# Performance work log

Hardware: AMD Instinct MI355X
Metric: run time of the kernel (lower is better)

The kernel has to match this reference:

```python
import jax, jax.numpy as jnp
import numpy as np

NEG = -1e6  # mask fill value used by d2l-style masked_softmax


def setup_inputs() -> dict:
    key = jax.random.key(0)
    kq, kk, kv, kl = jax.random.split(key, 4)
    B, Lq, Lk, D = 8, 2048, 2048, 64
    Q = jax.random.normal(kq, (B, Lq, D), dtype=jnp.float32)
    K = jax.random.normal(kk, (B, Lk, D), dtype=jnp.float32)
    V = jax.random.normal(kv, (B, Lk, D), dtype=jnp.float32)
    valid_len = jax.random.randint(kl, (B,), 1, Lk + 1, dtype=jnp.int64)
    return {"Q": Q, "K": K, "V": V, "valid_len": valid_len}


def reference(Q, K, V, valid_len):
    d = Q.shape[-1]
    scale = 1.0 / jnp.sqrt(jnp.asarray(d, dtype=Q.dtype))
    # scores: [B, Lq, Lk]
    S = jnp.einsum('bqd,bkd->bqk', Q, K) * scale
    Lk = K.shape[1]
    # per-batch key-length mask: position j valid iff j < valid_len[b]
    mask = jnp.arange(Lk)[None, None, :] < valid_len[:, None, None]
    S = jnp.where(mask, S, NEG)
    A = jax.nn.softmax(S, axis=-1)
    return jnp.einsum('bqk,bkd->bqd', A, V)
```

## Files before the change

### kernel.cpp

```cpp
#include <hip/hip_runtime.h>
#include <hip/hip_bf16.h>


constexpr int B_  = 8;
constexpr int L_  = 2048;
constexpr int D_  = 64;
constexpr int BQ  = 128;
constexpr int BK  = 64;
constexpr int LDK = 72;
constexpr int NQ  = L_ / BQ;

constexpr float QSCALE = 0.125f * 1.44269504088896340736f;

using bf16x8 = __attribute__((ext_vector_type(8))) __bf16;
using f32x4  = __attribute__((ext_vector_type(4))) float;

union frag_u { unsigned u[4]; bf16x8 v; };

#if __has_builtin(__builtin_amdgcn_exp2f)
#define EXP2(x) __builtin_amdgcn_exp2f(x)
#else
#define EXP2(x) exp2f(x)
#endif

__device__ __forceinline__ unsigned pack2(float lo, float hi) {
    __hip_bfloat162 h = __float22bfloat162_rn(make_float2(lo, hi));
    return *(unsigned*)&h;
}
__device__ __forceinline__ int sniff_valid(const int* vl, int b) {
    const int p1 = vl[1];
    return (p1 == 0) ? vl[2 * b] : vl[b];
}

__global__ __launch_bounds__(256, 3) void attn_fwd(
    const float* __restrict__ Q, const float* __restrict__ K,
    const float* __restrict__ V, const int* __restrict__ vl,
    float* __restrict__ O, float* __restrict__ Opart,
    float* __restrict__ lpart, int nsplit, int splitk)
{
    __shared__ __align__(16) unsigned short Ks[BK * LDK];
    __shared__ __align__(16) unsigned short Vt[D_ * LDK];
    __shared__ __align__(16) unsigned short Ps[4 * 32 * LDK];

    const int id   = blockIdx.x;
    const int qt   = id & (NQ - 1);
    const int b    = (id >> 4) & (B_ - 1);
    const int s    = id >> 7;
    const int tid  = threadIdx.x;
    const int wave = tid >> 6;
    const int lan  = tid & 15;
    const int quad = (tid >> 4) & 3;

    const int valid  = sniff_valid(vl, b);
    const int kstart = s * splitk;
    if (kstart >= valid) return;
    const int kend   = min(kstart + splitk, valid);
    const int ntiles = (kend - kstart + BK - 1) / BK;

    const float* Kg = K + (size_t)b * L_ * D_;
    const float* Vg = V + (size_t)b * L_ * D_;

    const int krow = tid >> 2, kc0 = (tid & 3) * 16;
    const int vk0  = (tid & 31) * 2, vd0 = (tid >> 5) * 8;

    float4 kr[4], vr[4];
    {
        const float* ks = Kg + (size_t)(kstart + krow) * D_ + kc0;
        #pragma unroll
        for (int p = 0; p < 4; ++p) kr[p] = *(const float4*)(ks + 4 * p);
        const float* vs = Vg + (size_t)(kstart + vk0) * D_ + vd0;
        vr[0] = *(const float4*)(vs);
        vr[1] = *(const float4*)(vs + 4);
        vr[2] = *(const float4*)(vs + D_);
        vr[3] = *(const float4*)(vs + D_ + 4);
    }

    bf16x8 aq[2][2];
    #pragma unroll
    for (int g = 0; g < 2; ++g) {
        const float* qs = Q + ((size_t)b * L_ + qt * BQ + wave * 32 + g * 16 + lan) * D_;
        float4 q0 = *(const float4*)(qs + quad * 8);
        float4 q1 = *(const float4*)(qs + quad * 8 + 4);
        float4 q2 = *(const float4*)(qs + 32 + quad * 8);
        float4 q3 = *(const float4*)(qs + 32 + quad * 8 + 4);
        frag_u f0, f1;
        f0.u[0] = pack2(q0.x * QSCALE, q0.y * QSCALE);
        f0.u[1] = pack2(q0.z * QSCALE, q0.w * QSCALE);
        f0.u[2] = pack2(q1.x * QSCALE, q1.y * QSCALE);
        f0.u[3] = pack2(q1.z * QSCALE, q1.w * QSCALE);
        f1.u[0] = pack2(q2.x * QSCALE, q2.y * QSCALE);
        f1.u[1] = pack2(q2.z * QSCALE, q2.w * QSCALE);
        f1.u[2] = pack2(q3.x * QSCALE, q3.y * QSCALE);
        f1.u[3] = pack2(q3.z * QSCALE, q3.w * QSCALE);
        aq[g][0] = f0.v;
        aq[g][1] = f1.v;
    }

    f32x4 oacc[2][4];
    #pragma unroll
    for (int g = 0; g < 2; ++g)
        #pragma unroll
        for (int c = 0; c < 4; ++c) oacc[g][c] = (f32x4){0.f, 0.f, 0.f, 0.f};
    float lsum[2] = {0.f, 0.f};

    unsigned short* Pw = &Ps[wave * 32 * LDK];

    for (int t = 0; t < ntiles; ++t) {
        const int kt = kstart + t * BK;
        __syncthreads();

        {
            unsigned us[8];
            #pragma unroll
            for (int p = 0; p < 4; ++p) {
                us[2*p]   = pack2(kr[p].x, kr[p].y);
                us[2*p+1] = pack2(kr[p].z, kr[p].w);
            }
            *(uint4*)&Ks[krow * LDK + kc0]     = *(uint4*)&us[0];
            *(uint4*)&Ks[krow * LDK + kc0 + 8] = *(uint4*)&us[4];
        }
        {
            const float* a = (const float*)&vr[0];
            const float* c = (const float*)&vr[2];
            #pragma unroll
            for (int j = 0; j < 8; ++j)
                *(unsigned*)&Vt[(vd0 + j) * LDK + vk0] = pack2(a[j], c[j]);
        }
        __syncthreads();

        if (t + 1 < ntiles) {
            const int kn = kt + BK;
            const float* ks = Kg + (size_t)(kn + krow) * D_ + kc0;
            #pragma unroll
            for (int p = 0; p < 4; ++p) kr[p] = *(const float4*)(ks + 4 * p);
            const float* vs = Vg + (size_t)(kn + vk0) * D_ + vd0;
            vr[0] = *(const float4*)(vs);
            vr[1] = *(const float4*)(vs + 4);
            vr[2] = *(const float4*)(vs + D_);
            vr[3] = *(const float4*)(vs + D_ + 4);
        }

        #pragma unroll
        for (int c = 0; c < 4; ++c) {
            bf16x8 ak0 = *(const bf16x8*)&Ks[(c*16 + lan) * LDK + quad * 8];
            bf16x8 ak1 = *(const bf16x8*)&Ks[(c*16 + lan) * LDK + 32 + quad * 8];
            f32x4 z0 = (f32x4){0.f, 0.f, 0.f, 0.f};
            f32x4 z1 = (f32x4){0.f, 0.f, 0.f, 0.f};
            z0 = __builtin_amdgcn_mfma_f32_16x16x32_bf16(ak0, aq[0][0], z0, 0, 0, 0);
            z1 = __builtin_amdgcn_mfma_f32_16x16x32_bf16(ak0, aq[1][0], z1, 0, 0, 0);
            z0 = __builtin_amdgcn_mfma_f32_16x16x32_bf16(ak1, aq[0][1], z0, 0, 0, 0);
            z1 = __builtin_amdgcn_mfma_f32_16x16x32_bf16(ak1, aq[1][1], z1, 0, 0, 0);

            const int kbase = kt + c * 16 + quad * 4;
            float p0[4], p1[4];
            #pragma unroll
            for (int r = 0; r < 4; ++r) {
                const bool ok = (kbase + r) < valid;
                p0[r] = ok ? EXP2(z0[r]) : 0.f;
                p1[r] = ok ? EXP2(z1[r]) : 0.f;
                lsum[0] += p0[r];
                lsum[1] += p1[r];
            }
            *(uint2*)&Pw[lan * LDK + c * 16 + quad * 4] =
                make_uint2(pack2(p0[0], p0[1]), pack2(p0[2], p0[3]));
            *(uint2*)&Pw[(16 + lan) * LDK + c * 16 + quad * 4] =
                make_uint2(pack2(p1[0], p1[1]), pack2(p1[2], p1[3]));
        }

        bf16x8 ap[2][2];
        #pragma unroll
        for (int g = 0; g < 2; ++g) {
            ap[g][0] = *(const bf16x8*)&Pw[(g*16 + lan) * LDK + quad * 8];
            ap[g][1] = *(const bf16x8*)&Pw[(g*16 + lan) * LDK + 32 + quad * 8];
        }
        #pragma unroll
        for (int c = 0; c < 4; ++c) {
            bf16x8 bv0 = *(const bf16x8*)&Vt[(c*16 + lan) * LDK + quad * 8];
            bf16x8 bv1 = *(const bf16x8*)&Vt[(c*16 + lan) * LDK + 32 + quad * 8];
            #pragma unroll
            for (int g = 0; g < 2; ++g) {
                oacc[g][c] = __builtin_amdgcn_mfma_f32_16x16x32_bf16(ap[g][0], bv0, oacc[g][c], 0, 0, 0);
                oacc[g][c] = __builtin_amdgcn_mfma_f32_16x16x32_bf16(ap[g][1], bv1, oacc[g][c], 0, 0, 0);
            }
        }
    }

    #pragma unroll
    for (int g = 0; g < 2; ++g) {
        lsum[g] += __shfl_xor(lsum[g], 16);
        lsum[g] += __shfl_xor(lsum[g], 32);
    }

    const int rowbase = qt * BQ + wave * 32;
    if (nsplit == 1) {
        #pragma unroll
        for (int g = 0; g < 2; ++g) {
            float inv[4];
            #pragma unroll
            for (int r = 0; r < 4; ++r)
                inv[r] = 1.0f / __shfl(lsum[g], quad * 4 + r);
            float* Og = O + ((size_t)b * L_ + rowbase + g * 16) * D_;
            #pragma unroll
            for (int c = 0; c < 4; ++c)
                #pragma unroll
                for (int r = 0; r < 4; ++r)
                    Og[(size_t)(quad * 4 + r) * D_ + c * 16 + lan] = oacc[g][c][r] * inv[r];
        }
    } else {
        #pragma unroll
        for (int g = 0; g < 2; ++g) {
            float* Og = Opart + ((size_t)s * B_ * L_ + (size_t)b * L_ + rowbase + g * 16) * D_;
            #pragma unroll
            for (int c = 0; c < 4; ++c)
                #pragma unroll
                for (int r = 0; r < 4; ++r)
                    Og[(size_t)(quad * 4 + r) * D_ + c * 16 + lan] = oacc[g][c][r];
            if (quad == 0)
                lpart[(size_t)s * B_ * L_ + (size_t)b * L_ + rowbase + g * 16 + lan] = lsum[g];
        }
    }
}

__global__ __launch_bounds__(256) void attn_combine(
    const float* __restrict__ Opart, const float* __restrict__ lpart,
    const int* __restrict__ vl, float* __restrict__ O,
    int nsplit, int splitk)
{
    const int idx = blockIdx.x * 256 + threadIdx.x;
    const int row = idx >> 4;
    const int b   = row >> 11;
    const int off = (idx & 15) * 4;
    const int valid = sniff_valid(vl, b);
    const int ns = min(nsplit, (valid + splitk - 1) / splitk);

    float Lsum = 0.f;
    float4 acc = make_float4(0.f, 0.f, 0.f, 0.f);
    for (int s = 0; s < ns; ++s) {
        Lsum += lpart[s * (B_ * L_) + row];
        float4 o4 = *(const float4*)&Opart[(size_t)s * (B_ * L_ * D_) + (size_t)row * D_ + off];
        acc.x += o4.x; acc.y += o4.y; acc.z += o4.z; acc.w += o4.w;
    }
    const float inv = 1.0f / Lsum;
    acc.x *= inv; acc.y *= inv; acc.z *= inv; acc.w *= inv;
    *(float4*)&O[(size_t)row * D_ + off] = acc;
}

extern "C" void kernel_launch(void* const* d_in, const int* in_sizes, int n_in,
                              void* d_out, int out_size, void* d_ws, size_t ws_size,
                              hipStream_t stream) {
    const float* Q  = (const float*)d_in[0];
    const float* K  = (const float*)d_in[1];
    const float* V  = (const float*)d_in[2];
    const int*   vl = (const int*)d_in[3];
    float* O = (float*)d_out;

    auto need = [](int n) {
        return (size_t)n * (B_ * L_ * D_ + B_ * L_) * sizeof(float);
    };
    int nsplit = 1;
    if      (ws_size >= need(4)) nsplit = 4;
    else if (ws_size >= need(2)) nsplit = 2;
    const int splitk = L_ / nsplit;

    float* Opart = (float*)d_ws;
    float* lpart = Opart + (size_t)nsplit * B_ * L_ * D_;

    attn_fwd<<<dim3(nsplit * B_ * NQ), 256, 0, stream>>>(
        Q, K, V, vl, O, Opart, lpart, nsplit, splitk);
    if (nsplit > 1)
        attn_combine<<<dim3((B_ * L_ * D_ / 4) / 256), 256, 0, stream>>>(
            Opart, lpart, vl, O, nsplit, splitk);
}
```

Measured before the change: 88.63 us.

## Fuse split-K combine into attention kernel via last-block atomic counter

Removes the separate combine kernel. Each split block writes its partial output and row sums, then bumps a per-tile atomic counter, and the last block to arrive reduces all splits and writes the final output. This saves one kernel launch and lets the reduction overlap with other blocks still computing. In exchange it adds a memset launch for the counters, thread fences, and a serialized reduction inside the final block of each tile.

Result: slower. 116.4 us (+31.4%).

```diff
diff --git a/kernel.cpp b/kernel.cpp
--- a/kernel.cpp
+++ b/kernel.cpp
@@ -36,11 +36,13 @@
     const float* __restrict__ Q, const float* __restrict__ K,
     const float* __restrict__ V, const int* __restrict__ vl,
     float* __restrict__ O, float* __restrict__ Opart,
-    float* __restrict__ lpart, int nsplit, int splitk)
+    float* __restrict__ lpart, int* __restrict__ cnt,
+    int nsplit, int splitk)
 {
     __shared__ __align__(16) unsigned short Ks[BK * LDK];
     __shared__ __align__(16) unsigned short Vt[D_ * LDK];
     __shared__ __align__(16) unsigned short Ps[4 * 32 * LDK];
+    __shared__ int last_flag;
 
     const int id   = blockIdx.x;
     const int qt   = id & (NQ - 1);
@@ -206,43 +208,48 @@
                 for (int r = 0; r < 4; ++r)
                     Og[(size_t)(quad * 4 + r) * D_ + c * 16 + lan] = oacc[g][c][r] * inv[r];
         }
-    } else {
-        #pragma unroll
-        for (int g = 0; g < 2; ++g) {
-            float* Og = Opart + ((size_t)s * B_ * L_ + (size_t)b * L_ + rowbase + g * 16) * D_;
-            #pragma unroll
-            for (int c = 0; c < 4; ++c)
-                #pragma unroll
-                for (int r = 0; r < 4; ++r)
-                    Og[(size_t)(quad * 4 + r) * D_ + c * 16 + lan] = oacc[g][c][r];
-            if (quad == 0)
-                lpart[(size_t)s * B_ * L_ + (size_t)b * L_ + rowbase + g * 16 + lan] = lsum[g];
-        }
-    }
-}
-
-__global__ __launch_bounds__(256) void attn_combine(
-    const float* __restrict__ Opart, const float* __restrict__ lpart,
-    const int* __restrict__ vl, float* __restrict__ O,
-    int nsplit, int splitk)
-{
-    const int idx = blockIdx.x * 256 + threadIdx.x;
-    const int row = idx >> 4;
-    const int b   = row >> 11;
-    const int off = (idx & 15) * 4;
-    const int valid = sniff_valid(vl, b);
+        return;
+    }
+
+    #pragma unroll
+    for (int g = 0; g < 2; ++g) {
+        float* Og = Opart + ((size_t)s * B_ * L_ + (size_t)b * L_ + rowbase + g * 16) * D_;
+        #pragma unroll
+        for (int c = 0; c < 4; ++c)
+            #pragma unroll
+            for (int r = 0; r < 4; ++r)
+                Og[(size_t)(quad * 4 + r) * D_ + c * 16 + lan] = oacc[g][c][r];
+        if (quad == 0)
+            lpart[(size_t)s * B_ * L_ + (size_t)b * L_ + rowbase + g * 16 + lan] = lsum[g];
+    }
+
     const int ns = min(nsplit, (valid + splitk - 1) / splitk);
-
-    float Lsum = 0.f;
-    float4 acc = make_float4(0.f, 0.f, 0.f, 0.f);
-    for (int s = 0; s < ns; ++s) {
-        Lsum += lpart[s * (B_ * L_) + row];
-        float4 o4 = *(const float4*)&Opart[(size_t)s * (B_ * L_ * D_) + (size_t)row * D_ + off];
-        acc.x += o4.x; acc.y += o4.y; acc.z += o4.z; acc.w += o4.w;
-    }
-    const float inv = 1.0f / Lsum;
-    acc.x *= inv; acc.y *= inv; acc.z *= inv; acc.w *= inv;
-    *(float4*)&O[(size_t)row * D_ + off] = acc;
+    __syncthreads();
+    if (tid == 0) {
+        __threadfence();
+        const int prev = atomicAdd(&cnt[b * NQ + qt], 1);
+        last_flag = (prev == ns - 1);
+    }
+    __syncthreads();
+    if (!last_flag) return;
+    __threadfence();
+
+    const size_t row0 = (size_t)b * L_ + qt * BQ;
+    for (int i = tid; i < BQ * (D_ / 4); i += 256) {
+        const int r   = i >> 4;
+        const int off = (i & 15) * 4;
+        const size_t row = row0 + r;
+        float Ls = 0.f;
+        float4 acc = make_float4(0.f, 0.f, 0.f, 0.f);
+        for (int s2 = 0; s2 < ns; ++s2) {
+            Ls += lpart[(size_t)s2 * (B_ * L_) + row];
+            float4 o4 = *(const float4*)&Opart[(size_t)s2 * (B_ * L_ * D_) + row * D_ + off];
+            acc.x += o4.x; acc.y += o4.y; acc.z += o4.z; acc.w += o4.w;
+        }
+        const float inv = 1.0f / Ls;
+        acc.x *= inv; acc.y *= inv; acc.z *= inv; acc.w *= inv;
+        *(float4*)&O[row * D_ + off] = acc;
+    }
 }
 
 extern "C" void kernel_launch(void* const* d_in, const int* in_sizes, int n_in,
@@ -255,7 +262,8 @@
     float* O = (float*)d_out;
 
     auto need = [](int n) {
-        return (size_t)n * (B_ * L_ * D_ + B_ * L_) * sizeof(float);
+        return (size_t)n * (B_ * L_ * D_ + B_ * L_) * sizeof(float)
+             + (size_t)(B_ * NQ) * sizeof(int);
     };
     int nsplit = 1;
     if      (ws_size >= need(4)) nsplit = 4;
@@ -264,10 +272,11 @@
 
     float* Opart = (float*)d_ws;
     float* lpart = Opart + (size_t)nsplit * B_ * L_ * D_;
+    int*   cnt   = (int*)(lpart + (size_t)nsplit * B_ * L_);
+
+    if (nsplit > 1)
+        hipMemsetAsync(cnt, 0, (size_t)(B_ * NQ) * sizeof(int), stream);
 
     attn_fwd<<<dim3(nsplit * B_ * NQ), 256, 0, stream>>>(
-        Q, K, V, vl, O, Opart, lpart, nsplit, splitk);
-    if (nsplit > 1)
-        attn_combine<<<dim3((B_ * L_ * D_ / 4) / 256), 256, 0, stream>>>(
-            Opart, lpart, vl, O, nsplit, splitk);
-}
+        Q, K, V, vl, O, Opart, lpart, cnt, nsplit, splitk);
+}
```
